# Optimization experiments

Hardware: AMD Instinct MI355X
Metric: run time of the kernel (lower is better)

Reference implementation:

```python
import jax, jax.numpy as jnp
import numpy as np

B, H, L, N_HEADS = 8192, 1024, 1024, 5

def setup_inputs() -> dict:
    key = jax.random.key(0)
    k1, k2, k3, k4, k5 = jax.random.split(key, 5)
    hidden_state = jax.random.normal(k1, (B, H), dtype=jnp.float32)
    W = jax.random.normal(k2, (N_HEADS, L, H), dtype=jnp.float32) * 0.02  # stacked head weights
    b = jax.random.normal(k3, (N_HEADS, L), dtype=jnp.float32) * 0.02     # stacked head biases
    group = jax.random.randint(k4, (B,), 0, 6, dtype=jnp.int32)
    labels = jax.random.randint(k5, (B,), 0, L, dtype=jnp.int32)
    return {"hidden_state": hidden_state, "W": W, "b": b, "group": group, "labels": labels}

def reference(hidden_state, W, b, group, labels):
    # 5 linear heads in one batched GEMM: [5, B, L]
    all_logits = jnp.einsum("bh,klh->kbl", hidden_state, W) + b[:, None, :]
    # per-row selection by group index (return_logit=True path)
    idx = jnp.clip(group, 0, N_HEADS - 1)
    sel = all_logits[idx, jnp.arange(B)]  # [B, L]
    # group == 5: row filled with broadcast label value (as in original)
    logits = jnp.where((group == 5)[:, None], labels[:, None].astype(jnp.float32), sel)
    return logits
```

## Files before the change

kernel.cpp:

```cpp
#include <hip/hip_runtime.h>
#include <stdint.h>

#define B_ROWS 8192
#define H_DIM 1024
#define L_DIM 1024
#define NH 5
#define YBLK 14

typedef short bf16x8 __attribute__((ext_vector_type(8)));
typedef float f32x4 __attribute__((ext_vector_type(4)));

typedef const __attribute__((address_space(1))) unsigned int* gas_uint_ptr;
typedef __attribute__((address_space(3))) unsigned int* las_uint_ptr;

__device__ __forceinline__ unsigned short f2bf(float f) {
  union { float f; unsigned int u; } v; v.f = f;
  return (unsigned short)((v.u + 0x7FFFu + ((v.u >> 16) & 1u)) >> 16);
}

__device__ __forceinline__ void load_lds16(const void* gsrc, void* ldst) {
  __builtin_amdgcn_global_load_lds((gas_uint_ptr)(uintptr_t)gsrc,
                                   (las_uint_ptr)(uintptr_t)ldst, 16, 0, 0);
}

__global__ void k_conv(const float* __restrict__ hidden, const float* __restrict__ W,
                       const int* __restrict__ group, const int* __restrict__ labels,
                       int* __restrict__ cnt, int* __restrict__ rowlist,
                       unsigned short* __restrict__ Hb, unsigned short* __restrict__ Wb,
                       float* __restrict__ out) {
  const int blk = blockIdx.x;
  const int t = threadIdx.x;
  if (blk < 512) {
    const f32x4* src = (const f32x4*)W;
    ushort4* dst = (ushort4*)Wb;
#pragma unroll
    for (int i = 0; i < 10; i++) {
      int idx = (i * 512 + blk) * 256 + t;
      f32x4 w = __builtin_nontemporal_load(&src[idx]);
      ushort4 o;
      o.x = f2bf(w.x); o.y = f2bf(w.y); o.z = f2bf(w.z); o.w = f2bf(w.w);
      dst[idx] = o;
    }
  } else if (blk < 1536) {
    const int rb = (blk - 512) * 8;
    int gs[8];
#pragma unroll
    for (int r = 0; r < 8; r++) gs[r] = group[rb + r];
#pragma unroll
    for (int r = 0; r < 8; r++) {
      int row = rb + r;
      if (gs[r] == NH) {
        float v = (float)labels[row];
        f32x4 fv; fv.x = v; fv.y = v; fv.z = v; fv.w = v;
        __builtin_nontemporal_store(fv, &((f32x4*)(out + (size_t)row * L_DIM))[t]);
      } else {
        f32x4 h = __builtin_nontemporal_load(&((const f32x4*)(hidden + (size_t)row * H_DIM))[t]);
        ushort4 o;
        o.x = f2bf(h.x); o.y = f2bf(h.y); o.z = f2bf(h.z); o.w = f2bf(h.w);
        ((ushort4*)(Hb + (size_t)row * H_DIM))[t] = o;
      }
    }
  } else {
    __shared__ int lcnt[NH];
    __shared__ int lbase[NH];
    if (t < NH) lcnt[t] = 0;
    __syncthreads();
    int b = (blk - 1536) * 256 + t;
    int g = group[b];
    int lpos = -1;
    if (g < NH) lpos = atomicAdd(&lcnt[g], 1);
    __syncthreads();
    if (t < NH) lbase[t] = atomicAdd(&cnt[t], lcnt[t]);
    __syncthreads();
    if (g < NH) rowlist[g * B_ROWS + lbase[g] + lpos] = b;
  }
}

__global__ __launch_bounds__(256, 2)
void k_gemm(const unsigned short* __restrict__ Hb, const unsigned short* __restrict__ Wb,
            const float* __restrict__ bias, const int* __restrict__ cnt,
            const int* __restrict__ rowlist, float* __restrict__ out) {
  const int wgid = blockIdx.x;
  const int xb = wgid & 7;
  const int m = wgid >> 3;
  const int yb = m % YBLK;
  const int head = m / YBLK;

  const int cntg = cnt[head];
  const int rowbase = yb * 128;
  if (rowbase >= cntg) return;
  const int n0 = xb * 128;

  __shared__ __align__(16) unsigned short As[2][128 * 64];
  __shared__ __align__(16) unsigned short Bs[2][128 * 64];

  const int t = threadIdx.x;
  const int wave = t >> 6, lane = t & 63;
  const int quad = lane >> 4, c16 = lane & 15;
  const int wm = (wave & 1) * 64, wn = (wave >> 1) * 64;

  const unsigned short* Wg = Wb + (size_t)head * L_DIM * H_DIM;
  const int* rl = rowlist + head * B_ROWS;

  const unsigned short* srcA[4];
  const unsigned short* srcB[4];
  int ldso[4];
#pragma unroll
  for (int p = 0; p < 4; p++) {
    int c = p * 256 + t;
    int row = c >> 3;
    int ks = ((c & 7) ^ (row & 7)) * 8;
    int idx = rowbase + row;
    idx = idx < cntg ? idx : cntg - 1;
    srcA[p] = Hb + (size_t)rl[idx] * H_DIM + ks;
    srcB[p] = Wg + (size_t)(n0 + row) * H_DIM + ks;
    ldso[p] = c * 8;
  }

  f32x4 acc[4][4] = {};

#pragma unroll
  for (int p = 0; p < 4; p++) {
    load_lds16(srcA[p], &As[0][ldso[p]]);
    load_lds16(srcB[p], &Bs[0][ldso[p]]);
  }
  __syncthreads();

  for (int kt = 0; kt < H_DIM; kt += 64) {
    const int cur = (kt >> 6) & 1;
    if (kt + 64 < H_DIM) {
      const int nxt = cur ^ 1;
#pragma unroll
      for (int p = 0; p < 4; p++) {
        load_lds16(srcA[p] + kt + 64, &As[nxt][ldso[p]]);
        load_lds16(srcB[p] + kt + 64, &Bs[nxt][ldso[p]]);
      }
    }
#pragma unroll
    for (int kk = 0; kk < 64; kk += 32) {
      bf16x8 af[4], bf[4];
      const int sw = c16 & 7;
      const int colb = (kk >> 4) << 1;
      const int cl = (colb + quad) ^ sw;
#pragma unroll
      for (int i = 0; i < 4; i++) {
        int row = wm + i * 16 + c16;
        af[i] = *(const bf16x8*)(&As[cur][row * 64 + cl * 8]);
      }
#pragma unroll
      for (int j = 0; j < 4; j++) {
        int row = wn + j * 16 + c16;
        bf[j] = *(const bf16x8*)(&Bs[cur][row * 64 + cl * 8]);
      }
#pragma unroll
      for (int i = 0; i < 4; i++)
#pragma unroll
        for (int j = 0; j < 4; j++)
          acc[i][j] = __builtin_amdgcn_mfma_f32_16x16x32_bf16(af[i], bf[j], acc[i][j], 0, 0, 0);
    }
    __syncthreads();
  }

  float bv[4];
#pragma unroll
  for (int j = 0; j < 4; j++) bv[j] = bias[head * L_DIM + n0 + wn + j * 16 + c16];
#pragma unroll
  for (int i = 0; i < 4; i++) {
    int rloc0 = wm + i * 16 + quad * 4;
#pragma unroll
    for (int r = 0; r < 4; r++) {
      int idx = rloc0 + r;
      if (rowbase + idx < cntg) {
        int orow = rl[rowbase + idx];
        float* orowp = out + (size_t)orow * L_DIM + n0 + wn;
#pragma unroll
        for (int j = 0; j < 4; j++)
          __builtin_nontemporal_store(acc[i][j][r] + bv[j], &orowp[j * 16 + c16]);
      }
    }
  }
}

extern "C" void kernel_launch(void* const* d_in, const int* in_sizes, int n_in,
                              void* d_out, int out_size, void* d_ws, size_t ws_size,
                              hipStream_t stream) {
  const float* hidden = (const float*)d_in[0];
  const float* W      = (const float*)d_in[1];
  const float* bias   = (const float*)d_in[2];
  const int* group    = (const int*)d_in[3];
  const int* labels   = (const int*)d_in[4];
  float* out = (float*)d_out;

  char* ws = (char*)d_ws;
  int* cnt = (int*)ws;
  int* rowlist = (int*)(ws + 256);
  unsigned short* Wb = (unsigned short*)(ws + (1 << 18));
  unsigned short* Hb = (unsigned short*)(ws + (1 << 18) + (size_t)NH * L_DIM * H_DIM * 2);

  (void)hipMemsetAsync(cnt, 0, 64, stream);
  k_conv<<<1568, 256, 0, stream>>>(hidden, W, group, labels, cnt, rowlist, Hb, Wb, out);
  k_gemm<<<8 * YBLK * NH, 256, 0, stream>>>(Hb, Wb, bias, cnt, rowlist, out);
}
```

Before: 129.5 us.

## Triple-buffer GEMM K-loop with 32-wide tiles and single barrier per step

New measurement: 144.9 us. +11.9%, slower.

```diff
diff --git a/kernel.cpp b/kernel.cpp
--- a/kernel.cpp
+++ b/kernel.cpp
@@ -91,8 +91,8 @@
   if (rowbase >= cntg) return;
   const int n0 = xb * 128;
 
-  __shared__ __align__(16) unsigned short As[2][128 * 64];
-  __shared__ __align__(16) unsigned short Bs[2][128 * 64];
+  __shared__ __align__(16) unsigned short As[3][128 * 32];
+  __shared__ __align__(16) unsigned short Bs[3][128 * 32];
 
   const int t = threadIdx.x;
   const int wave = t >> 6, lane = t & 63;
@@ -102,14 +102,14 @@
   const unsigned short* Wg = Wb + (size_t)head * L_DIM * H_DIM;
   const int* rl = rowlist + head * B_ROWS;
 
-  const unsigned short* srcA[4];
-  const unsigned short* srcB[4];
-  int ldso[4];
-#pragma unroll
-  for (int p = 0; p < 4; p++) {
+  const unsigned short* srcA[2];
+  const unsigned short* srcB[2];
+  int ldso[2];
+#pragma unroll
+  for (int p = 0; p < 2; p++) {
     int c = p * 256 + t;
-    int row = c >> 3;
-    int ks = ((c & 7) ^ (row & 7)) * 8;
+    int row = c >> 2;
+    int ks = ((c & 3) ^ (row & 3)) * 8;
     int idx = rowbase + row;
     idx = idx < cntg ? idx : cntg - 1;
     srcA[p] = Hb + (size_t)rl[idx] * H_DIM + ks;
@@ -119,47 +119,57 @@
 
   f32x4 acc[4][4] = {};
 
-#pragma unroll
-  for (int p = 0; p < 4; p++) {
-    load_lds16(srcA[p], &As[0][ldso[p]]);
-    load_lds16(srcB[p], &Bs[0][ldso[p]]);
-  }
-  __syncthreads();
-
-  for (int kt = 0; kt < H_DIM; kt += 64) {
-    const int cur = (kt >> 6) & 1;
-    if (kt + 64 < H_DIM) {
-      const int nxt = cur ^ 1;
-#pragma unroll
-      for (int p = 0; p < 4; p++) {
-        load_lds16(srcA[p] + kt + 64, &As[nxt][ldso[p]]);
-        load_lds16(srcB[p] + kt + 64, &Bs[nxt][ldso[p]]);
-      }
-    }
-#pragma unroll
-    for (int kk = 0; kk < 64; kk += 32) {
-      bf16x8 af[4], bf[4];
-      const int sw = c16 & 7;
-      const int colb = (kk >> 4) << 1;
-      const int cl = (colb + quad) ^ sw;
-#pragma unroll
-      for (int i = 0; i < 4; i++) {
-        int row = wm + i * 16 + c16;
-        af[i] = *(const bf16x8*)(&As[cur][row * 64 + cl * 8]);
-      }
-#pragma unroll
-      for (int j = 0; j < 4; j++) {
-        int row = wn + j * 16 + c16;
-        bf[j] = *(const bf16x8*)(&Bs[cur][row * 64 + cl * 8]);
-      }
-#pragma unroll
-      for (int i = 0; i < 4; i++)
-#pragma unroll
-        for (int j = 0; j < 4; j++)
-          acc[i][j] = __builtin_amdgcn_mfma_f32_16x16x32_bf16(af[i], bf[j], acc[i][j], 0, 0, 0);
-    }
-    __syncthreads();
-  }
+#define STAGE(buf, kt)                                      \
+  {                                                         \
+    load_lds16(srcA[0] + (kt), &As[buf][ldso[0]]);          \
+    load_lds16(srcB[0] + (kt), &Bs[buf][ldso[0]]);          \
+    load_lds16(srcA[1] + (kt), &As[buf][ldso[1]]);          \
+    load_lds16(srcB[1] + (kt), &Bs[buf][ldso[1]]);          \
+  }
+
+  const int cl = quad ^ (c16 & 3);
+
+#define COMPUTE(sbuf)                                                     \
+  {                                                                       \
+    bf16x8 af[4], bf[4];                                                  \
+    _Pragma("unroll")                                                     \
+    for (int i = 0; i < 4; i++)                                           \
+      af[i] = *(const bf16x8*)(&As[sbuf][(wm + i * 16 + c16) * 32 + cl * 8]); \
+    _Pragma("unroll")                                                     \
+    for (int j = 0; j < 4; j++)                                           \
+      bf[j] = *(const bf16x8*)(&Bs[sbuf][(wn + j * 16 + c16) * 32 + cl * 8]); \
+    __builtin_amdgcn_s_setprio(1);                                        \
+    _Pragma("unroll")                                                     \
+    for (int i = 0; i < 4; i++)                                           \
+      _Pragma("unroll")                                                   \
+      for (int j = 0; j < 4; j++)                                         \
+        acc[i][j] = __builtin_amdgcn_mfma_f32_16x16x32_bf16(af[i], bf[j], \
+                                                            acc[i][j], 0, 0, 0); \
+    __builtin_amdgcn_s_setprio(0);                                        \
+  }
+
+  STAGE(0, 0)
+  STAGE(1, 32)
+
+  int s = 0;
+  for (int kt = 0; kt < 30; ++kt) {
+    asm volatile("s_waitcnt vmcnt(4)" ::: "memory");
+    __builtin_amdgcn_s_barrier();
+    __builtin_amdgcn_sched_barrier(0);
+    int s2 = s + 2; if (s2 >= 3) s2 -= 3;
+    STAGE(s2, (kt + 2) * 32)
+    COMPUTE(s)
+    s = (s + 1 == 3) ? 0 : s + 1;
+  }
+  asm volatile("s_waitcnt vmcnt(4)" ::: "memory");
+  __builtin_amdgcn_s_barrier();
+  __builtin_amdgcn_sched_barrier(0);
+  COMPUTE(s)
+  s = (s + 1 == 3) ? 0 : s + 1;
+  asm volatile("s_waitcnt vmcnt(0)" ::: "memory");
+  __builtin_amdgcn_s_barrier();
+  __builtin_amdgcn_sched_barrier(0);
+  COMPUTE(s)
 
   float bv[4];
 #pragma unroll
@@ -179,6 +189,8 @@
       }
     }
   }
+#undef STAGE
+#undef COMPUTE
 }
 
 extern "C" void kernel_launch(void* const* d_in, const int* in_sizes, int n_in,
```
